# Optimization experiments

Measured on AMD Instinct MI355X. Metric: run time of the kernel, lower is better.

Reference implementation:

```python
import jax, jax.numpy as jnp
import numpy as np

NEG_INF = -1e9


def setup_inputs() -> dict:
    key = jax.random.key(0)
    k1, k2, k3, k4, k5, k6 = jax.random.split(key, 6)
    B, P, N, C, H = 32, 512, 64, 9, 128
    polylines = jax.random.normal(k1, (B, P, N, C), dtype=jnp.float32)
    polylines_mask = jax.random.uniform(k2, (B, P, N)) > 0.1
    # MLP params (Linear(C,H) -> ReLU -> Linear(H,H)), torch-style init scale
    W1 = jax.random.uniform(k3, (C, H), minval=-1.0, maxval=1.0) / jnp.sqrt(C)
    b1 = jax.random.uniform(k4, (H,), minval=-1.0, maxval=1.0) / jnp.sqrt(C)
    W2 = jax.random.uniform(k5, (H, H), minval=-1.0, maxval=1.0) / jnp.sqrt(H)
    b2 = jax.random.uniform(k6, (H,), minval=-1.0, maxval=1.0) / jnp.sqrt(H)
    return {"polylines": polylines, "polylines_mask": polylines_mask,
            "W1": W1, "b1": b1, "W2": W2, "b2": b2}


def reference(polylines, polylines_mask, W1, b1, W2, b2):
    # Point MLP applied to all points (invalid ones are overwritten below,
    # identical math to the torch masked-gather version).
    h = jax.nn.relu(jnp.einsum('bpnc,ch->bpnh', polylines, W1) + b1)
    feat = jnp.einsum('bpnh,hd->bpnd', h, W2) + b2  # [B,P,N,H]
    feat = jnp.where(polylines_mask[..., None], feat, NEG_INF)
    pooled = jnp.max(feat, axis=2)  # [B,P,H]
    # Polylines with no valid points pooled to NEG_INF -> zero them out.
    any_valid = jnp.any(polylines_mask, axis=2)  # [B,P]
    return jnp.where(any_valid[..., None], pooled, 0.0)
```

## Files before the change

### kernel.cpp

```cpp
#include <hip/hip_runtime.h>


using bf16x8 = __attribute__((ext_vector_type(8))) short;
using f32x4  = __attribute__((ext_vector_type(4))) float;
using u16x4  = __attribute__((ext_vector_type(4))) unsigned short;

#define MFMA_BF16(A,B,C) __builtin_amdgcn_mfma_f32_16x16x32_bf16((A),(B),(C),0,0,0)

__device__ __forceinline__ unsigned short f2bf(float f) {
  union { float f; unsigned int u; } v; v.f = f;
  unsigned int r = v.u + 0x7fffu + ((v.u >> 16) & 1u);
  return (unsigned short)(r >> 16);
}

__global__ void prep_kernel(const float* __restrict__ W1, const float* __restrict__ W2,
                            const void* __restrict__ mask,
                            unsigned short* __restrict__ w1t, unsigned short* __restrict__ w2t,
                            int* __restrict__ flag) {
  int b = blockIdx.x, t = threadIdx.x;
  if (b < 68) {
    int idx = b * 256 + t;
    if (idx < 128 * 136) {
      int d = idx / 136, h = idx - d * 136;
      float v = (h < 128) ? W2[h * 128 + d] : 0.f;
      w2t[idx] = f2bf(v);
    }
  } else if (b < 88) {
    int idx = (b - 68) * 256 + t;
    if (idx < 128 * 40) {
      int h = idx / 40, c = idx - h * 40;
      float v = (c < 9) ? W1[c * 128 + h] : 0.f;
      w1t[idx] = f2bf(v);
    }
  } else {
    __shared__ int cnt;
    if (t == 0) cnt = 0;
    __syncthreads();
    const unsigned char* mb = (const unsigned char*)mask;
    int local = 0;
    for (int i = t * 16; i < t * 16 + 16; i++) local += (mb[i] != 0) ? 1 : 0;
    atomicAdd(&cnt, local);
    __syncthreads();
    if (t == 0) *flag = (cnt > 2800) ? 1 : 0;
  }
}

__global__ __launch_bounds__(256, 3) void poly_main_k(
    const float* __restrict__ X, const void* __restrict__ mask,
    const float* __restrict__ b1g, const float* __restrict__ b2g,
    const unsigned short* __restrict__ w1t, const unsigned short* __restrict__ w2t,
    const int* __restrict__ flagp, float* __restrict__ out)
{
  union SU { unsigned short Xs[128 * 40]; float P[2 * 16 * 132]; };
  __shared__ __align__(16) SU su;
  __shared__ __align__(16) unsigned short Hb[128 * 136];
  __shared__ float maskf[128];

  const int tid  = threadIdx.x;
  const int lane = tid & 63;
  const int w    = tid >> 6;
  const int wr   = w >> 1, wc = w & 1;
  const int li   = lane & 15, q = lane >> 4;

  {
    unsigned int* xz = (unsigned int*)su.Xs;
    #pragma unroll
    for (int i = 0; i < 10; i++) xz[tid + i * 256] = 0u;
  }
  __syncthreads();
  {
    const float* xb = X + (long long)blockIdx.x * (128 * 9);
    for (int i = tid; i < 1152; i += 256) {
      int m = i / 9, c = i - m * 9;
      su.Xs[m * 40 + c] = f2bf(xb[i]);
    }
    int flag = *flagp;
    if (tid < 128) {
      long long gi = (long long)blockIdx.x * 128 + tid;
      int valid;
      if (flag) valid = (((const unsigned char*)mask)[gi] != 0);
      else      valid = (((const int*)mask)[gi] != 0);
      maskf[tid] = valid ? 0.f : -4e9f;
    }
  }
  __syncthreads();

  f32x4 acc1[4][4];
  #pragma unroll
  for (int a = 0; a < 4; a++)
    #pragma unroll
    for (int b = 0; b < 4; b++) acc1[a][b] = f32x4{0.f, 0.f, 0.f, 0.f};
  {
    bf16x8 af[4], bf[4];
    #pragma unroll
    for (int th = 0; th < 4; th++)
      af[th] = *(const bf16x8*)(w1t + (wr * 64 + th * 16 + li) * 40 + q * 8);
    #pragma unroll
    for (int tm = 0; tm < 4; tm++)
      bf[tm] = *(const bf16x8*)(su.Xs + (wc * 64 + tm * 16 + li) * 40 + q * 8);
    #pragma unroll
    for (int th = 0; th < 4; th++)
      #pragma unroll
      for (int tm = 0; tm < 4; tm++)
        acc1[th][tm] = MFMA_BF16(af[th], bf[tm], acc1[th][tm]);
  }
  #pragma unroll
  for (int th = 0; th < 4; th++) {
    f32x4 bv = *(const f32x4*)(b1g + wr * 64 + th * 16 + q * 4);
    #pragma unroll
    for (int tm = 0; tm < 4; tm++) {
      int m = wc * 64 + tm * 16 + li;
      u16x4 hv;
      #pragma unroll
      for (int r = 0; r < 4; r++) {
        float v = acc1[th][tm][r] + bv[r];
        v = fmaxf(v, 0.f);
        hv[r] = f2bf(v);
      }
      *(u16x4*)(Hb + m * 136 + wr * 64 + th * 16 + q * 4) = hv;
    }
  }
  __syncthreads();

  f32x4 acc2[4][4];
  #pragma unroll
  for (int a = 0; a < 4; a++)
    #pragma unroll
    for (int b = 0; b < 4; b++) acc2[a][b] = f32x4{0.f, 0.f, 0.f, 0.f};
  #pragma unroll
  for (int ks = 0; ks < 4; ks++) {
    bf16x8 af[4], bf[4];
    #pragma unroll
    for (int td = 0; td < 4; td++)
      af[td] = *(const bf16x8*)(w2t + (wr * 64 + td * 16 + li) * 136 + ks * 32 + q * 8);
    #pragma unroll
    for (int tm = 0; tm < 4; tm++)
      bf[tm] = *(const bf16x8*)(Hb + (wc * 64 + tm * 16 + li) * 136 + ks * 32 + q * 8);
    #pragma unroll
    for (int td = 0; td < 4; td++)
      #pragma unroll
      for (int tm = 0; tm < 4; tm++)
        acc2[td][tm] = MFMA_BF16(af[td], bf[tm], acc2[td][tm]);
  }

  {
    float mf[4];
    #pragma unroll
    for (int tm = 0; tm < 4; tm++) mf[tm] = maskf[wc * 64 + tm * 16 + li];
    #pragma unroll
    for (int td = 0; td < 4; td++) {
      f32x4 bv = *(const f32x4*)(b2g + wr * 64 + td * 16 + q * 4);
      f32x4 pooled;
      #pragma unroll
      for (int r = 0; r < 4; r++) {
        float v0 = acc2[td][0][r] + bv[r] + mf[0];
        float v1 = acc2[td][1][r] + bv[r] + mf[1];
        float v2 = acc2[td][2][r] + bv[r] + mf[2];
        float v3 = acc2[td][3][r] + bv[r] + mf[3];
        pooled[r] = fmaxf(fmaxf(v0, v1), fmaxf(v2, v3));
      }
      *(f32x4*)(su.P + (wc * 16 + li) * 132 + wr * 64 + td * 16 + q * 4) = pooled;
    }
  }
  __syncthreads();

  {
    int p = tid >> 7, d = tid & 127;
    const float* Pp = su.P + p * 16 * 132 + d;
    float v = Pp[0];
    #pragma unroll
    for (int j = 1; j < 16; j++) v = fmaxf(v, Pp[j * 132]);
    if (v < -1e8f) v = 0.f;
    out[(long long)blockIdx.x * 256 + tid] = v;
  }
}

extern "C" void kernel_launch(void* const* d_in, const int* in_sizes, int n_in,
                              void* d_out, int out_size, void* d_ws, size_t ws_size,
                              hipStream_t stream) {
  const float* X    = (const float*)d_in[0];
  const void*  mask = d_in[1];
  const float* W1   = (const float*)d_in[2];
  const float* b1   = (const float*)d_in[3];
  const float* W2   = (const float*)d_in[4];
  const float* b2   = (const float*)d_in[5];
  float* out = (float*)d_out;

  unsigned short* w1t = (unsigned short*)d_ws;
  unsigned short* w2t = w1t + 128 * 40;
  int* flag = (int*)((char*)d_ws + 45056);

  prep_kernel<<<89, 256, 0, stream>>>(W1, W2, mask, w1t, w2t, flag);
  poly_main_k<<<8192, 256, 0, stream>>>(X, mask, b1, b2, w1t, w2t, flag, out);
}
```

Before: 156.7 us.

## Load X and mask directly into registers and pool via wave shuffles

Each lane now builds its MFMA B-operand straight from global X and reads its mask values straight from global memory, so the LDS staging buffers for X, the mask and the partial maxima are gone along with two barriers. The final max over points uses xor-shuffles within the wave instead of an LDS round trip. The bias add is moved after the max, bf16 packing switches to a perm-based round-half-up helper, and the occupancy hint rises to 4 blocks per CU. The costs are uncoalesced strided global loads of X, extra shuffle instructions, and slightly different bf16 rounding on ties.

```diff
diff --git a/kernel.cpp b/kernel.cpp
--- a/kernel.cpp
+++ b/kernel.cpp
@@ -3,7 +3,6 @@
 
 using bf16x8 = __attribute__((ext_vector_type(8))) short;
 using f32x4  = __attribute__((ext_vector_type(4))) float;
-using u16x4  = __attribute__((ext_vector_type(4))) unsigned short;
 
 #define MFMA_BF16(A,B,C) __builtin_amdgcn_mfma_f32_16x16x32_bf16((A),(B),(C),0,0,0)
 
@@ -11,6 +10,11 @@
   union { float f; unsigned int u; } v; v.f = f;
   unsigned int r = v.u + 0x7fffu + ((v.u >> 16) & 1u);
   return (unsigned short)(r >> 16);
+}
+
+__device__ __forceinline__ unsigned int pack_bf2(float a, float b) {
+  union { float f; unsigned int u; } ua, ub; ua.f = a; ub.f = b;
+  return __builtin_amdgcn_perm(ub.u + 0x8000u, ua.u + 0x8000u, 0x07060302u);
 }
 
 __global__ void prep_kernel(const float* __restrict__ W1, const float* __restrict__ W2,
@@ -45,16 +49,13 @@
   }
 }
 
-__global__ __launch_bounds__(256, 3) void poly_main_k(
+__global__ __launch_bounds__(256, 4) void poly_main_k(
     const float* __restrict__ X, const void* __restrict__ mask,
     const float* __restrict__ b1g, const float* __restrict__ b2g,
     const unsigned short* __restrict__ w1t, const unsigned short* __restrict__ w2t,
     const int* __restrict__ flagp, float* __restrict__ out)
 {
-  union SU { unsigned short Xs[128 * 40]; float P[2 * 16 * 132]; };
-  __shared__ __align__(16) SU su;
   __shared__ __align__(16) unsigned short Hb[128 * 136];
-  __shared__ float maskf[128];
 
   const int tid  = threadIdx.x;
   const int lane = tid & 63;
@@ -62,28 +63,41 @@
   const int wr   = w >> 1, wc = w & 1;
   const int li   = lane & 15, q = lane >> 4;
 
+  float mf[4];
   {
-    unsigned int* xz = (unsigned int*)su.Xs;
-    #pragma unroll
-    for (int i = 0; i < 10; i++) xz[tid + i * 256] = 0u;
-  }
-  __syncthreads();
+    int flag = *flagp;
+    long long mbase = (long long)blockIdx.x * 128 + wc * 64 + li;
+    if (flag) {
+      const unsigned char* mp = (const unsigned char*)mask;
+      #pragma unroll
+      for (int tm = 0; tm < 4; tm++) mf[tm] = mp[mbase + tm * 16] ? 0.f : -4e9f;
+    } else {
+      const int* mp = (const int*)mask;
+      #pragma unroll
+      for (int tm = 0; tm < 4; tm++) mf[tm] = mp[mbase + tm * 16] ? 0.f : -4e9f;
+    }
+  }
+
+  bf16x8 bx[4];
   {
     const float* xb = X + (long long)blockIdx.x * (128 * 9);
-    for (int i = tid; i < 1152; i += 256) {
-      int m = i / 9, c = i - m * 9;
-      su.Xs[m * 40 + c] = f2bf(xb[i]);
-    }
-    int flag = *flagp;
-    if (tid < 128) {
-      long long gi = (long long)blockIdx.x * 128 + tid;
-      int valid;
-      if (flag) valid = (((const unsigned char*)mask)[gi] != 0);
-      else      valid = (((const int*)mask)[gi] != 0);
-      maskf[tid] = valid ? 0.f : -4e9f;
-    }
-  }
-  __syncthreads();
+    #pragma unroll
+    for (int tm = 0; tm < 4; tm++) {
+      int m = wc * 64 + tm * 16 + li;
+      const float* xr = xb + m * 9;
+      union { bf16x8 v; unsigned int u[4]; } uu;
+      uu.u[0] = uu.u[1] = uu.u[2] = uu.u[3] = 0u;
+      if (q == 0) {
+        uu.u[0] = pack_bf2(xr[0], xr[1]);
+        uu.u[1] = pack_bf2(xr[2], xr[3]);
+        uu.u[2] = pack_bf2(xr[4], xr[5]);
+        uu.u[3] = pack_bf2(xr[6], xr[7]);
+      } else if (q == 1) {
+        uu.u[0] = pack_bf2(xr[8], 0.f);
+      }
+      bx[tm] = uu.v;
+    }
+  }
 
   f32x4 acc1[4][4];
   #pragma unroll
@@ -91,33 +105,31 @@
     #pragma unroll
     for (int b = 0; b < 4; b++) acc1[a][b] = f32x4{0.f, 0.f, 0.f, 0.f};
   {
-    bf16x8 af[4], bf[4];
+    bf16x8 af[4];
     #pragma unroll
     for (int th = 0; th < 4; th++)
       af[th] = *(const bf16x8*)(w1t + (wr * 64 + th * 16 + li) * 40 + q * 8);
     #pragma unroll
-    for (int tm = 0; tm < 4; tm++)
-      bf[tm] = *(const bf16x8*)(su.Xs + (wc * 64 + tm * 16 + li) * 40 + q * 8);
-    #pragma unroll
     for (int th = 0; th < 4; th++)
       #pragma unroll
       for (int tm = 0; tm < 4; tm++)
-        acc1[th][tm] = MFMA_BF16(af[th], bf[tm], acc1[th][tm]);
-  }
+        acc1[th][tm] = MFMA_BF16(af[th], bx[tm], acc1[th][tm]);
+  }
+
   #pragma unroll
   for (int th = 0; th < 4; th++) {
     f32x4 bv = *(const f32x4*)(b1g + wr * 64 + th * 16 + q * 4);
     #pragma unroll
     for (int tm = 0; tm < 4; tm++) {
       int m = wc * 64 + tm * 16 + li;
-      u16x4 hv;
-      #pragma unroll
-      for (int r = 0; r < 4; r++) {
-        float v = acc1[th][tm][r] + bv[r];
-        v = fmaxf(v, 0.f);
-        hv[r] = f2bf(v);
-      }
-      *(u16x4*)(Hb + m * 136 + wr * 64 + th * 16 + q * 4) = hv;
+      float v0 = fmaxf(acc1[th][tm][0] + bv[0], 0.f);
+      float v1 = fmaxf(acc1[th][tm][1] + bv[1], 0.f);
+      float v2 = fmaxf(acc1[th][tm][2] + bv[2], 0.f);
+      float v3 = fmaxf(acc1[th][tm][3] + bv[3], 0.f);
+      uint2 hv;
+      hv.x = pack_bf2(v0, v1);
+      hv.y = pack_bf2(v2, v3);
+      *(uint2*)(Hb + m * 136 + wr * 64 + th * 16 + q * 4) = hv;
     }
   }
   __syncthreads();
@@ -143,35 +155,41 @@
         acc2[td][tm] = MFMA_BF16(af[td], bf[tm], acc2[td][tm]);
   }
 
-  {
-    float mf[4];
-    #pragma unroll
-    for (int tm = 0; tm < 4; tm++) mf[tm] = maskf[wc * 64 + tm * 16 + li];
+  f32x4 pooled[4];
+  #pragma unroll
+  for (int td = 0; td < 4; td++) {
+    f32x4 bv = *(const f32x4*)(b2g + wr * 64 + td * 16 + q * 4);
+    #pragma unroll
+    for (int r = 0; r < 4; r++) {
+      float v0 = acc2[td][0][r] + mf[0];
+      float v1 = acc2[td][1][r] + mf[1];
+      float v2 = acc2[td][2][r] + mf[2];
+      float v3 = acc2[td][3][r] + mf[3];
+      pooled[td][r] = fmaxf(fmaxf(v0, v1), fmaxf(v2, v3)) + bv[r];
+    }
+  }
+
+  #pragma unroll
+  for (int s = 8; s >= 1; s >>= 1) {
     #pragma unroll
     for (int td = 0; td < 4; td++) {
-      f32x4 bv = *(const f32x4*)(b2g + wr * 64 + td * 16 + q * 4);
-      f32x4 pooled;
       #pragma unroll
       for (int r = 0; r < 4; r++) {
-        float v0 = acc2[td][0][r] + bv[r] + mf[0];
-        float v1 = acc2[td][1][r] + bv[r] + mf[1];
-        float v2 = acc2[td][2][r] + bv[r] + mf[2];
-        float v3 = acc2[td][3][r] + bv[r] + mf[3];
-        pooled[r] = fmaxf(fmaxf(v0, v1), fmaxf(v2, v3));
+        float o = __shfl_xor(pooled[td][r], s, 64);
+        pooled[td][r] = fmaxf(pooled[td][r], o);
       }
-      *(f32x4*)(su.P + (wc * 16 + li) * 132 + wr * 64 + td * 16 + q * 4) = pooled;
-    }
-  }
-  __syncthreads();
-
-  {
-    int p = tid >> 7, d = tid & 127;
-    const float* Pp = su.P + p * 16 * 132 + d;
-    float v = Pp[0];
-    #pragma unroll
-    for (int j = 1; j < 16; j++) v = fmaxf(v, Pp[j * 132]);
-    if (v < -1e8f) v = 0.f;
-    out[(long long)blockIdx.x * 256 + tid] = v;
+    }
+  }
+
+  if (li == 0) {
+    long long poly = (long long)blockIdx.x * 2 + wc;
+    #pragma unroll
+    for (int td = 0; td < 4; td++) {
+      f32x4 v = pooled[td];
+      #pragma unroll
+      for (int r = 0; r < 4; r++) if (v[r] < -1e8f) v[r] = 0.f;
+      *(f32x4*)(out + poly * 128 + wr * 64 + td * 16 + q * 4) = v;
+    }
   }
 }
 
```

Result: slower. 168.1 us (+7.3%).
